# Performance work log

Measured on AMD Instinct MI355X. Metric: run time of the kernel, lower is better.

Reference implementation:

```python
import jax, jax.numpy as jnp
import numpy as np

DIM = 128
WIN = (2, 7, 7)
HEADS = 4
N = WIN[0] * WIN[1] * WIN[2]  # 98
B_ = 2048
NW = 256  # num windows per sample; B_ // NW = batch = 8


def _relative_position_index(win):
    t = np.arange(win[0]); h = np.arange(win[1]); w = np.arange(win[2])
    coords = np.stack(np.meshgrid(t, h, w, indexing='ij'))  # (3, T, H, W)
    cf = coords.reshape(3, -1)  # (3, N)
    rel = cf[:, :, None] - cf[:, None, :]  # (3, N, N)
    rel = rel.transpose(1, 2, 0).copy()
    rel[:, :, 0] += win[0] - 1
    rel[:, :, 1] += win[1] - 1
    rel[:, :, 2] += win[2] - 1
    rel[:, :, 0] *= (2 * win[1] - 1) * (2 * win[2] - 1)
    rel[:, :, 1] *= 2 * win[2] - 1
    return rel.sum(-1).astype(np.int32)  # (N, N)


def setup_inputs() -> dict:
    key = jax.random.key(0)
    ks = jax.random.split(key, 8)
    table_len = (2 * WIN[0] - 1) * (2 * WIN[1] - 1) * (2 * WIN[2] - 1)  # 507
    x = jax.random.normal(ks[0], (B_, N, DIM), dtype=jnp.float32)
    # 0 / -inf style additive mask (use -1e4 as finite -inf)
    u = jax.random.uniform(ks[1], (NW, N, N))
    mask = jnp.where(u < 0.9, 0.0, -1e4).astype(jnp.float32)
    qkv_w = jax.random.normal(ks[2], (3 * DIM, DIM), dtype=jnp.float32) * (DIM ** -0.5)
    qkv_b = jax.random.normal(ks[3], (3 * DIM,), dtype=jnp.float32) * 0.02
    proj_w = jax.random.normal(ks[4], (DIM, DIM), dtype=jnp.float32) * (DIM ** -0.5)
    proj_b = jax.random.normal(ks[5], (DIM,), dtype=jnp.float32) * 0.02
    bias_table = jax.random.normal(ks[6], (table_len, HEADS), dtype=jnp.float32) * 0.02
    rel_index = jnp.asarray(_relative_position_index(WIN))
    return {"x": x, "mask": mask, "qkv_w": qkv_w, "qkv_b": qkv_b,
            "proj_w": proj_w, "proj_b": proj_b, "bias_table": bias_table,
            "rel_index": rel_index}


def reference(x, mask, qkv_w, qkv_b, proj_w, proj_b, bias_table, rel_index):
    Bq, n, c = x.shape
    hd = c // HEADS
    scale = hd ** -0.5
    qkv = x @ qkv_w.T + qkv_b  # (B_, N, 3C)
    qkv = qkv.reshape(Bq, n, 3, HEADS, hd).transpose(2, 0, 3, 1, 4)  # (3, B_, H, N, hd)
    q, k, v = qkv[0] * scale, qkv[1], qkv[2]
    attn = jnp.einsum('bhnd,bhmd->bhnm', q, k)  # (B_, H, N, N)
    bias = bias_table[rel_index.reshape(-1)].reshape(n, n, HEADS)
    attn = attn + bias.transpose(2, 0, 1)[None]  # add (1, H, N, N)
    nW = mask.shape[0]
    attn = attn.reshape(Bq // nW, nW, HEADS, n, n) + mask[None, :, None]
    attn = jax.nn.softmax(attn.reshape(Bq, HEADS, n, n), axis=-1)
    out = jnp.einsum('bhnm,bhmd->bhnd', attn, v)  # (B_, H, N, hd)
    out = out.transpose(0, 2, 1, 3).reshape(Bq, n, c)
    return out @ proj_w.T + proj_b
```

## Files before the change

### kernel.cpp

```cpp
#include <hip/hip_runtime.h>
#include <hip/hip_bf16.h>


#define NTOK 98
#define NN (NTOK * NTOK)
#define SCALE 0.17677669529663687f
#define LOG2E 1.4426950408889634f

typedef short bf16x8 __attribute__((ext_vector_type(8)));
typedef float f32x4 __attribute__((ext_vector_type(4)));
#define MFMA(a, b, c) __builtin_amdgcn_mfma_f32_16x16x32_bf16(a, b, c, 0, 0, 0)

static __device__ __forceinline__ unsigned short f2bf(float f) {
  union { float f; unsigned int i; } x; x.f = f;
  unsigned int u = x.i;
  unsigned int rnd = ((u >> 16) & 1u) + 0x7fffu;
  return (unsigned short)((u + rnd) >> 16);
}

static __device__ __forceinline__ unsigned int cvt_pk_bf16(float lo, float hi) {
  unsigned int pk;
  asm("v_cvt_pk_bf16_f32 %0, %1, %2" : "=v"(pk) : "v"(lo), "v"(hi));
  return pk;
}

__global__ void k0_w(const float* __restrict__ qkv_w, const float* __restrict__ proj_w,
                     unsigned short* __restrict__ wqb, unsigned short* __restrict__ wpb) {
  int idx = blockIdx.x * 256 + threadIdx.x;
  if (idx < 49152) wqb[idx] = f2bf(qkv_w[idx]);
  else wpb[idx - 49152] = f2bf(proj_w[idx - 49152]);
}

__global__ void k0b_bm(const float* __restrict__ table, const int* __restrict__ rel,
                       const float* __restrict__ mask, float* __restrict__ bm) {
  const int wmodh = blockIdx.x, mt = blockIdx.y;
  const int wmod = wmodh >> 2, h = wmodh & 3;
  float* dst = bm + (size_t)(wmodh * 7 + mt) * 1792;
  for (int i = threadIdx.x; i < 1792; i += 256) {
    int reg = i & 3, lane = (i >> 2) & 63, nt = i >> 8;
    int quad = lane >> 4, L15 = lane & 15;
    int row = mt * 16 + quad * 4 + reg;
    int col = nt * 16 + L15;
    float v = -1.0e30f;
    if (row < NTOK && col < NTOK) {
      int nm = row * NTOK + col;
      v = (table[rel[nm] * 4 + h] + mask[(size_t)wmod * NN + nm]) * LOG2E;
    }
    dst[i] = v;
  }
}

__global__ __launch_bounds__(256) void k1_qkv(const float* __restrict__ x,
                                              const unsigned short* __restrict__ wqb,
                                              const float* __restrict__ qkv_b,
                                              unsigned short* __restrict__ q,
                                              unsigned short* __restrict__ k,
                                              unsigned short* __restrict__ v) {
  __shared__ unsigned short xt[64 * 136];
  __shared__ unsigned short wt[128 * 136];
  const int t = threadIdx.x;
  const int r0 = blockIdx.x * 64;
  const int wv = t >> 6, lane = t & 63, L15 = lane & 15, quad = lane >> 4;

#pragma unroll
  for (int i = 0; i < 8; ++i) {
    int idx = t + (i << 8);
    int row = idx >> 5, c4 = idx & 31;
    float4 xv = *(const float4*)&x[(size_t)(r0 + row) * 128 + c4 * 4];
    ushort4 pk; pk.x = f2bf(xv.x); pk.y = f2bf(xv.y); pk.z = f2bf(xv.z); pk.w = f2bf(xv.w);
    *(ushort4*)&xt[row * 136 + c4 * 4] = pk;
  }

  bf16x8 af[4];
  bool afLoaded = false;

  for (int g = 0; g < 3; ++g) {
    if (g) __syncthreads();
#pragma unroll
    for (int i = 0; i < 8; ++i) {
      int idx = t + (i << 8);
      int c = idx >> 4, kq = idx & 15;
      *(uint4*)&wt[c * 136 + kq * 8] = ((const uint4*)wqb)[g * 2048 + idx];
    }
    __syncthreads();
    if (!afLoaded) {
      afLoaded = true;
#pragma unroll
      for (int kt = 0; kt < 4; ++kt)
        af[kt] = *(const bf16x8*)&xt[(wv * 16 + L15) * 136 + kt * 32 + quad * 8];
    }

    f32x4 acc[8];
#pragma unroll
    for (int nt = 0; nt < 8; ++nt) {
      f32x4 a = {0.f, 0.f, 0.f, 0.f};
#pragma unroll
      for (int kt = 0; kt < 4; ++kt) {
        bf16x8 bf_ = *(const bf16x8*)&wt[(nt * 16 + L15) * 136 + kt * 32 + quad * 8];
        a = MFMA(af[kt], bf_, a);
      }
      acc[nt] = a;
    }

    unsigned short* dst = (g == 0) ? q : ((g == 1) ? k : v);
    const float sc = (g == 0) ? (SCALE * LOG2E) : 1.0f;
    float bsc[8];
#pragma unroll
    for (int nt = 0; nt < 8; ++nt) bsc[nt] = qkv_b[g * 128 + nt * 16 + L15] * sc;
#pragma unroll
    for (int reg = 0; reg < 4; ++reg) {
      int R = r0 + wv * 16 + quad * 4 + reg;
      int b = R / NTOK, n = R - b * NTOK;
      size_t base0 = ((size_t)b * 4 * NTOK + n) * 32;
#pragma unroll
      for (int h2 = 0; h2 < 4; ++h2) {
        float v0 = acc[2 * h2][reg] * sc + bsc[2 * h2];
        float v1 = acc[2 * h2 + 1][reg] * sc + bsc[2 * h2 + 1];
        unsigned int pk = cvt_pk_bf16(v0, v1);
        unsigned short* dp = dst + base0 + (size_t)h2 * (NTOK * 32) + L15;
        dp[0]  = (unsigned short)pk;
        dp[16] = (unsigned short)(pk >> 16);
      }
    }
  }
}

__global__ __launch_bounds__(256) void k2_attn(const unsigned short* __restrict__ qg,
                                               const unsigned short* __restrict__ kg,
                                               const unsigned short* __restrict__ vg,
                                               const float* __restrict__ bm,
                                               unsigned short* __restrict__ og) {
  __shared__ unsigned short sK[112 * 40];
  __shared__ unsigned short sVt[32 * 136];
  __shared__ unsigned short sP[4 * 16 * 136];
  const int t = threadIdx.x;
  const int bh = blockIdx.x, bw = bh >> 2, h = bh & 3;
  const int wmodh = ((bw & 255) << 2) + h;
  const size_t base = (size_t)bh * (NTOK * 32);
  const int wv = t >> 6, lane = t & 63, L15 = lane & 15, quad = lane >> 4;
  unsigned short* myP = sP + wv * (16 * 136);

  for (int i = t; i < 2240; i += 256) ((unsigned int*)sK)[i] = 0;
  for (int j = lane; j < 128; j += 64) {
    int r = j >> 3, cp = j & 7;
    *(unsigned int*)&myP[r * 136 + 112 + cp * 2] = 0;
  }
  __syncthreads();
  for (int i = t; i < 392; i += 256) {
    int row = i >> 2, kq = i & 3;
    *(uint4*)&sK[row * 40 + kq * 8] = ((const uint4*)kg)[(size_t)bh * 392 + i];
  }
  for (int i = t; i < 392; i += 256) {
    uint4 w = ((const uint4*)vg)[(size_t)bh * 392 + i];
    int n = i >> 2, d0 = (i & 3) << 3;
    const unsigned short* pw = (const unsigned short*)&w;
#pragma unroll
    for (int j = 0; j < 8; ++j) sVt[(d0 + j) * 136 + n] = pw[j];
  }
  __syncthreads();

  auto strip = [&](int mt) {
    const float* bmp = bm + (size_t)(wmodh * 7 + mt) * 1792 + (lane << 2);
    bf16x8 aq = *(const bf16x8*)&qg[base + (size_t)(mt * 16 + L15) * 32 + quad * 8];
    f32x4 s[7];
#pragma unroll
    for (int nt = 0; nt < 7; ++nt) {
      f32x4 c = *(const f32x4*)&bmp[nt << 8];
      bf16x8 bk = *(const bf16x8*)&sK[(nt * 16 + L15) * 40 + quad * 8];
      s[nt] = MFMA(aq, bk, c);
    }
    float rsv[4];
#pragma unroll
    for (int reg = 0; reg < 4; ++reg) {
      float sum = 0.f;
#pragma unroll
      for (int nt = 0; nt < 7; ++nt) {
        float e = __builtin_amdgcn_exp2f(s[nt][reg]);
        s[nt][reg] = e; sum += e;
      }
#pragma unroll
      for (int d = 1; d < 16; d <<= 1) sum += __shfl_xor(sum, d, 64);
      rsv[reg] = __builtin_amdgcn_rcpf(sum);
      unsigned short* pr = myP + (quad * 4 + reg) * 136 + L15;
#pragma unroll
      for (int p = 0; p < 4; ++p) {
        int n1 = (p < 3) ? 2 * p + 1 : 2 * p;
        unsigned int pk = cvt_pk_bf16(s[2 * p][reg], s[n1][reg]);
        pr[2 * p * 16] = (unsigned short)pk;
        if (p < 3) pr[n1 * 16] = (unsigned short)(pk >> 16);
      }
    }
    f32x4 o0 = {0.f, 0.f, 0.f, 0.f}, o1 = {0.f, 0.f, 0.f, 0.f};
#pragma unroll
    for (int kt = 0; kt < 4; ++kt) {
      bf16x8 ap  = *(const bf16x8*)&myP[L15 * 136 + kt * 32 + quad * 8];
      bf16x8 bv0 = *(const bf16x8*)&sVt[L15 * 136 + kt * 32 + quad * 8];
      bf16x8 bv1 = *(const bf16x8*)&sVt[(16 + L15) * 136 + kt * 32 + quad * 8];
      o0 = MFMA(ap, bv0, o0);
      o1 = MFMA(ap, bv1, o1);
    }
#pragma unroll
    for (int reg = 0; reg < 4; ++reg) {
      int n = mt * 16 + quad * 4 + reg;
      if (n < NTOK) {
        size_t ob = ((size_t)bw * NTOK + n) * 128 + h * 32;
        float a0 = o0[reg] * rsv[reg], a1 = o1[reg] * rsv[reg];
        unsigned int pk = cvt_pk_bf16(a0, a1);
        og[ob + L15]      = (unsigned short)pk;
        og[ob + 16 + L15] = (unsigned short)(pk >> 16);
      }
    }
  };
  strip(wv * 2);
  if (wv < 3) strip(wv * 2 + 1);
}

__global__ __launch_bounds__(256) void k3_proj(const unsigned short* __restrict__ og,
                                               const unsigned short* __restrict__ wpb,
                                               const float* __restrict__ pb,
                                               float* __restrict__ out) {
  __shared__ unsigned short ot[64 * 136];
  __shared__ unsigned short wt[128 * 136];
  const int t = threadIdx.x;
  const int r0 = blockIdx.x * 64;
  const int wv = t >> 6, lane = t & 63, L15 = lane & 15, quad = lane >> 4;

#pragma unroll
  for (int i = 0; i < 4; ++i) {
    int idx = t + (i << 8);
    int row = idx >> 4, kq = idx & 15;
    *(uint4*)&ot[row * 136 + kq * 8] = ((const uint4*)og)[(size_t)(r0 + row) * 16 + kq];
  }
#pragma unroll
  for (int i = 0; i < 8; ++i) {
    int idx = t + (i << 8);
    int c = idx >> 4, kq = idx & 15;
    *(uint4*)&wt[c * 136 + kq * 8] = ((const uint4*)wpb)[idx];
  }
  __syncthreads();

  bf16x8 af[4];
#pragma unroll
  for (int kt = 0; kt < 4; ++kt)
    af[kt] = *(const bf16x8*)&ot[(wv * 16 + L15) * 136 + kt * 32 + quad * 8];

  f32x4 acc[8];
#pragma unroll
  for (int nt = 0; nt < 8; ++nt) {
    f32x4 a = {0.f, 0.f, 0.f, 0.f};
#pragma unroll
    for (int kt = 0; kt < 4; ++kt) {
      bf16x8 bf_ = *(const bf16x8*)&wt[(nt * 16 + L15) * 136 + kt * 32 + quad * 8];
      a = MFMA(af[kt], bf_, a);
    }
    acc[nt] = a;
  }

  float bias[8];
#pragma unroll
  for (int nt = 0; nt < 8; ++nt) bias[nt] = pb[nt * 16 + L15];
#pragma unroll
  for (int reg = 0; reg < 4; ++reg) {
    size_t R = (size_t)(r0 + wv * 16 + quad * 4 + reg);
#pragma unroll
    for (int nt = 0; nt < 8; ++nt)
      out[R * 128 + nt * 16 + L15] = acc[nt][reg] + bias[nt];
  }
}

extern "C" void kernel_launch(void* const* d_in, const int* in_sizes, int n_in,
                              void* d_out, int out_size, void* d_ws, size_t ws_size,
                              hipStream_t stream) {
  (void)in_sizes; (void)n_in; (void)out_size; (void)ws_size;
  const float* x      = (const float*)d_in[0];
  const float* mask   = (const float*)d_in[1];
  const float* qkv_w  = (const float*)d_in[2];
  const float* qkv_b  = (const float*)d_in[3];
  const float* proj_w = (const float*)d_in[4];
  const float* proj_b = (const float*)d_in[5];
  const float* table  = (const float*)d_in[6];
  const int*   rel    = (const int*)d_in[7];
  float* out = (float*)d_out;

  const size_t QS = (size_t)2048 * 4 * NTOK * 32;
  unsigned short* q   = (unsigned short*)d_ws;
  unsigned short* k   = q + QS;
  unsigned short* v   = k + QS;
  unsigned short* o   = v + QS;
  unsigned short* wqb = o + QS;
  unsigned short* wpb = wqb + 49152;
  float* bm = (float*)d_out;

  k0_w<<<256, 256, 0, stream>>>(qkv_w, proj_w, wqb, wpb);
  k0b_bm<<<dim3(1024, 7), 256, 0, stream>>>(table, rel, mask, bm);
  k1_qkv<<<200704 / 64, 256, 0, stream>>>(x, wqb, qkv_b, q, k, v);
  k2_attn<<<2048 * 4, 256, 0, stream>>>(q, k, v, bm, o);
  k3_proj<<<200704 / 64, 256, 0, stream>>>(o, wpb, proj_b, out);
}
```

Measured before the change: 374.2 us.

## Persist attention blocks per window-head, keep bias-mask in registers as bf16, prefetch K/V

The attention kernel now launches one block per (window-mod, head) and loops over the 8 batch samples that share that mask. The bias+mask tile is loaded once into registers and reused across all 8. The bias+mask buffer is stored as packed bf16 to halve its traffic. K/V for the next iteration are prefetched into registers while the current one computes, and the transposed V tile in shared memory uses an XOR swizzle to reduce bank conflicts. The costs are fewer blocks (1024), so less parallelism, more register pressure from the extra launch-bounds constraint, and lower precision in the additive bias/mask.

```diff
diff --git a/kernel.cpp b/kernel.cpp
--- a/kernel.cpp
+++ b/kernel.cpp
@@ -32,21 +32,26 @@
 }
 
 __global__ void k0b_bm(const float* __restrict__ table, const int* __restrict__ rel,
-                       const float* __restrict__ mask, float* __restrict__ bm) {
+                       const float* __restrict__ mask, unsigned int* __restrict__ bm) {
   const int wmodh = blockIdx.x, mt = blockIdx.y;
   const int wmod = wmodh >> 2, h = wmodh & 3;
-  float* dst = bm + (size_t)(wmodh * 7 + mt) * 1792;
-  for (int i = threadIdx.x; i < 1792; i += 256) {
-    int reg = i & 3, lane = (i >> 2) & 63, nt = i >> 8;
+  unsigned int* dst = bm + (size_t)(wmodh * 7 + mt) * 896;
+  for (int u = threadIdx.x; u < 896; u += 256) {
+    int w = u & 1, lane = (u >> 1) & 63, nt = u >> 7;
     int quad = lane >> 4, L15 = lane & 15;
-    int row = mt * 16 + quad * 4 + reg;
     int col = nt * 16 + L15;
-    float v = -1.0e30f;
-    if (row < NTOK && col < NTOK) {
-      int nm = row * NTOK + col;
-      v = (table[rel[nm] * 4 + h] + mask[(size_t)wmod * NN + nm]) * LOG2E;
-    }
-    dst[i] = v;
+    unsigned int pk = 0;
+#pragma unroll
+    for (int rr = 0; rr < 2; ++rr) {
+      int row = mt * 16 + quad * 4 + 2 * w + rr;
+      float v = -1.0e30f;
+      if (row < NTOK && col < NTOK) {
+        int nm = row * NTOK + col;
+        v = (table[rel[nm] * 4 + h] + mask[(size_t)wmod * NN + nm]) * LOG2E;
+      }
+      pk |= ((unsigned int)f2bf(v)) << (16 * rr);
+    }
+    dst[u] = pk;
   }
 }
 
@@ -125,47 +130,64 @@
   }
 }
 
-__global__ __launch_bounds__(256) void k2_attn(const unsigned short* __restrict__ qg,
-                                               const unsigned short* __restrict__ kg,
-                                               const unsigned short* __restrict__ vg,
-                                               const float* __restrict__ bm,
-                                               unsigned short* __restrict__ og) {
+__global__ __launch_bounds__(256, 4) void k2_attn(const unsigned short* __restrict__ qg,
+                                                  const unsigned short* __restrict__ kg,
+                                                  const unsigned short* __restrict__ vg,
+                                                  const unsigned int* __restrict__ bm16,
+                                                  unsigned short* __restrict__ og) {
   __shared__ unsigned short sK[112 * 40];
   __shared__ unsigned short sVt[32 * 136];
   __shared__ unsigned short sP[4 * 16 * 136];
   const int t = threadIdx.x;
-  const int bh = blockIdx.x, bw = bh >> 2, h = bh & 3;
-  const int wmodh = ((bw & 255) << 2) + h;
-  const size_t base = (size_t)bh * (NTOK * 32);
+  const int wmodh = blockIdx.x;
+  const int wmod = wmodh >> 2, h = wmodh & 3;
   const int wv = t >> 6, lane = t & 63, L15 = lane & 15, quad = lane >> 4;
   unsigned short* myP = sP + wv * (16 * 136);
 
-  for (int i = t; i < 2240; i += 256) ((unsigned int*)sK)[i] = 0;
+  for (int i = t; i < 280; i += 256) ((unsigned int*)sK)[1960 + i] = 0;
   for (int j = lane; j < 128; j += 64) {
     int r = j >> 3, cp = j & 7;
     *(unsigned int*)&myP[r * 136 + 112 + cp * 2] = 0;
   }
-  __syncthreads();
-  for (int i = t; i < 392; i += 256) {
-    int row = i >> 2, kq = i & 3;
-    *(uint4*)&sK[row * 40 + kq * 8] = ((const uint4*)kg)[(size_t)bh * 392 + i];
-  }
-  for (int i = t; i < 392; i += 256) {
-    uint4 w = ((const uint4*)vg)[(size_t)bh * 392 + i];
-    int n = i >> 2, d0 = (i & 3) << 3;
-    const unsigned short* pw = (const unsigned short*)&w;
-#pragma unroll
-    for (int j = 0; j < 8; ++j) sVt[(d0 + j) * 136 + n] = pw[j];
-  }
-  __syncthreads();
-
-  auto strip = [&](int mt) {
-    const float* bmp = bm + (size_t)(wmodh * 7 + mt) * 1792 + (lane << 2);
-    bf16x8 aq = *(const bf16x8*)&qg[base + (size_t)(mt * 16 + L15) * 32 + quad * 8];
+  for (int i = t; i < 32 * 30; i += 256) {
+    int d = i / 30, nl = 98 + i % 30;
+    int swz = ((d >> 3) & 3) << 3;
+    sVt[d * 136 + (nl ^ swz)] = 0;
+  }
+
+  const int s0 = wv * 2, s1 = wv * 2 + 1;
+  uint2 bmA[7], bmB[7];
+  {
+    const uint2* p0 = (const uint2*)(bm16 + (size_t)(wmodh * 7 + s0) * 896);
+#pragma unroll
+    for (int nt = 0; nt < 7; ++nt) bmA[nt] = p0[nt * 64 + lane];
+    if (wv < 3) {
+      const uint2* p1 = (const uint2*)(bm16 + (size_t)(wmodh * 7 + s1) * 896);
+#pragma unroll
+      for (int nt = 0; nt < 7; ++nt) bmB[nt] = p1[nt * 64 + lane];
+    }
+  }
+
+  const int i0 = t, i1 = t + 256;
+  uint4 rk0, rk1, rv0, rv1;
+  auto loadKV = [&](int bh) {
+    const uint4* kp = (const uint4*)kg + (size_t)bh * 392;
+    const uint4* vp = (const uint4*)vg + (size_t)bh * 392;
+    rk0 = kp[i0]; rv0 = vp[i0];
+    if (i1 < 392) { rk1 = kp[i1]; rv1 = vp[i1]; }
+  };
+  loadKV(wmod * 4 + h);
+
+  auto strip = [&](int mt, const uint2* bmp, bf16x8 aq, int bw) {
     f32x4 s[7];
 #pragma unroll
     for (int nt = 0; nt < 7; ++nt) {
-      f32x4 c = *(const f32x4*)&bmp[nt << 8];
+      uint2 pkb = bmp[nt];
+      f32x4 c;
+      c[0] = __uint_as_float(pkb.x << 16);
+      c[1] = __uint_as_float(pkb.x & 0xffff0000u);
+      c[2] = __uint_as_float(pkb.y << 16);
+      c[3] = __uint_as_float(pkb.y & 0xffff0000u);
       bf16x8 bk = *(const bf16x8*)&sK[(nt * 16 + L15) * 40 + quad * 8];
       s[nt] = MFMA(aq, bk, c);
     }
@@ -190,12 +212,15 @@
         if (p < 3) pr[n1 * 16] = (unsigned short)(pk >> 16);
       }
     }
+    const int sw0 = (L15 >> 3) << 3;
+    const int sw1 = (((16 + L15) >> 3) & 3) << 3;
     f32x4 o0 = {0.f, 0.f, 0.f, 0.f}, o1 = {0.f, 0.f, 0.f, 0.f};
 #pragma unroll
     for (int kt = 0; kt < 4; ++kt) {
-      bf16x8 ap  = *(const bf16x8*)&myP[L15 * 136 + kt * 32 + quad * 8];
-      bf16x8 bv0 = *(const bf16x8*)&sVt[L15 * 136 + kt * 32 + quad * 8];
-      bf16x8 bv1 = *(const bf16x8*)&sVt[(16 + L15) * 136 + kt * 32 + quad * 8];
+      int cb = kt * 32 + quad * 8;
+      bf16x8 ap  = *(const bf16x8*)&myP[L15 * 136 + cb];
+      bf16x8 bv0 = *(const bf16x8*)&sVt[L15 * 136 + (cb ^ sw0)];
+      bf16x8 bv1 = *(const bf16x8*)&sVt[(16 + L15) * 136 + (cb ^ sw1)];
       o0 = MFMA(ap, bv0, o0);
       o1 = MFMA(ap, bv1, o1);
     }
@@ -211,8 +236,41 @@
       }
     }
   };
-  strip(wv * 2);
-  if (wv < 3) strip(wv * 2 + 1);
+
+  for (int it = 0; it < 8; ++it) {
+    const int bw = wmod + (it << 8);
+    const int bh = bw * 4 + h;
+    const size_t base = (size_t)bh * (NTOK * 32);
+
+    if (it) __syncthreads();
+    {
+      int row = i0 >> 2, kq = i0 & 3;
+      *(uint4*)&sK[row * 40 + kq * 8] = rk0;
+      int n = i0 >> 2, d0 = (i0 & 3) << 3;
+      int swz = ((d0 >> 3) & 3) << 3;
+      const unsigned short* pw = (const unsigned short*)&rv0;
+#pragma unroll
+      for (int j = 0; j < 8; ++j) sVt[(d0 + j) * 136 + (n ^ swz)] = pw[j];
+      if (i1 < 392) {
+        int row1 = i1 >> 2, kq1 = i1 & 3;
+        *(uint4*)&sK[row1 * 40 + kq1 * 8] = rk1;
+        int n_ = i1 >> 2, d0_ = (i1 & 3) << 3;
+        int swz_ = ((d0_ >> 3) & 3) << 3;
+        const unsigned short* pw1 = (const unsigned short*)&rv1;
+#pragma unroll
+        for (int j = 0; j < 8; ++j) sVt[(d0_ + j) * 136 + (n_ ^ swz_)] = pw1[j];
+      }
+    }
+    __syncthreads();
+    if (it < 7) loadKV((bw + 256) * 4 + h);
+
+    bf16x8 aqA = *(const bf16x8*)&qg[base + (size_t)(s0 * 16 + L15) * 32 + quad * 8];
+    bf16x8 aqB;
+    if (wv < 3) aqB = *(const bf16x8*)&qg[base + (size_t)(s1 * 16 + L15) * 32 + quad * 8];
+
+    strip(s0, bmA, aqA, bw);
+    if (wv < 3) strip(s1, bmB, aqB, bw);
+  }
 }
 
 __global__ __launch_bounds__(256) void k3_proj(const unsigned short* __restrict__ og,
@@ -289,11 +347,11 @@
   unsigned short* o   = v + QS;
   unsigned short* wqb = o + QS;
   unsigned short* wpb = wqb + 49152;
-  float* bm = (float*)d_out;
+  unsigned int* bm = (unsigned int*)d_out;
 
   k0_w<<<256, 256, 0, stream>>>(qkv_w, proj_w, wqb, wpb);
   k0b_bm<<<dim3(1024, 7), 256, 0, stream>>>(table, rel, mask, bm);
   k1_qkv<<<200704 / 64, 256, 0, stream>>>(x, wqb, qkv_b, q, k, v);
-  k2_attn<<<2048 * 4, 256, 0, stream>>>(q, k, v, bm, o);
+  k2_attn<<<1024, 256, 0, stream>>>(q, k, v, bm, o);
   k3_proj<<<200704 / 64, 256, 0, stream>>>(o, wpb, proj_b, out);
 }
```

New measurement: 370.9 us. Within noise of the previous version (-0.9%).
